# Kernel optimization log

Measured on AMD Instinct MI355X. Metric: run time of the kernel, lower is better.

Reference implementation:

```python
import jax, jax.numpy as jnp
import numpy as np

ALPHA = 0.9        # LIF membrane decay
THRESH = 1.0       # spike threshold
SURR_BETA = 4.0    # surrogate-gradient sharpness
TIME_STEPS = 32    # fabric simulation steps per token position


def _spike(v):
    """Heaviside spike with sigmoid surrogate gradient (straight-through)."""
    hard = (v >= THRESH).astype(v.dtype)
    soft = jax.nn.sigmoid(SURR_BETA * (v - THRESH))
    return soft + jax.lax.stop_gradient(hard - soft)


def setup_inputs() -> dict:
    key = jax.random.key(0)
    k0, k1, k2, k3 = jax.random.split(key, 4)
    B, S, D = 8, 128, 512
    N_in, N_out = 1024, 1024
    embeddings = jax.random.normal(k0, (B, S, D), jnp.float32)
    W_in = jax.random.normal(k1, (D, N_in), jnp.float32) / np.sqrt(D).astype(np.float32)
    b_in = jnp.zeros((N_in,), jnp.float32)
    W_conn = jax.random.normal(k2, (N_in, N_out), jnp.float32) / np.sqrt(N_in).astype(np.float32)
    W_out = jax.random.normal(k3, (N_out, D), jnp.float32) / np.sqrt(N_out).astype(np.float32)
    b_out = jnp.zeros((D,), jnp.float32)
    return {"embeddings": embeddings, "W_in": W_in, "b_in": b_in,
            "W_conn": W_conn, "W_out": W_out, "b_out": b_out}


def reference(embeddings, W_in, b_in, W_conn, W_out, b_out):
    B, S, D = embeddings.shape
    N_in = W_in.shape[1]
    N_out = W_conn.shape[1]

    # embed_to_snn + relu, precomputed for all positions: [B, S, N_in]
    snn_input = jax.nn.relu(jnp.einsum('bsd,dn->bsn', embeddings, W_in) + b_in)

    def time_step(carry, _):
        v_in, v_out, pos_input = carry
        # input population: leaky integrate external current
        v_in = ALPHA * v_in + pos_input
        s_in = _spike(v_in)
        v_in = v_in - s_in * THRESH          # soft reset
        # output population: driven by input-population spikes
        v_out = ALPHA * v_out + s_in @ W_conn
        s_out = _spike(v_out)
        v_out = v_out - s_out * THRESH
        n_spk = jax.lax.stop_gradient(s_in.sum() + s_out.sum())
        return (v_in, v_out, pos_input), (s_out, n_spk)

    def pos_step(carry, pos_input):
        v_in, v_out = carry
        (v_in, v_out, _), (s_outs, n_spks) = jax.lax.scan(
            time_step, (v_in, v_out, pos_input), None, length=TIME_STEPS)
        spike_acc = s_outs.sum(axis=0)       # [B, N_out], sum over timesteps
        pos_out = spike_acc @ W_out + b_out  # snn_to_embed
        return (v_in, v_out), (pos_out, n_spks.sum())

    v0_in = jnp.zeros((B, N_in), embeddings.dtype)
    v0_out = jnp.zeros((B, N_out), embeddings.dtype)
    snn_seq = jnp.swapaxes(snn_input, 0, 1)  # [S, B, N_in]: scan over positions
    _, (outs, spk_counts) = jax.lax.scan(pos_step, (v0_in, v0_out), snn_seq)

    output_embeddings = jnp.swapaxes(outs, 0, 1)  # [B, S, D]
    total_neurons = N_in + N_out
    spike_rate = spk_counts.sum() / (B * S * total_neurons * TIME_STEPS)
    return output_embeddings, spike_rate
```

## Files before the change

### kernel.cpp

```cpp
#include <hip/hip_runtime.h>
#include <stdint.h>

#define B 8
#define S 128
#define D 512
#define NIN 1024
#define NOUT 1024
#define T 32

typedef __attribute__((ext_vector_type(8))) short short8;
typedef __attribute__((ext_vector_type(4))) float floatx4;

__global__ __launch_bounds__(256) void k_gemm(const float* __restrict__ A,
                                              const float* __restrict__ Bm,
                                              const float* __restrict__ bias,
                                              float* __restrict__ C,
                                              int M, int N, int K, int relu)
{
    __shared__ float As[16][64];
    __shared__ float Bs[16][64];
    const int tid = threadIdx.x;
    const int bx = blockIdx.x, by = blockIdx.y;
    const int tx = tid & 15, ty = tid >> 4;
    const int ar = tid >> 2, ak = (tid & 3) << 2;
    const int bk = tid >> 4, bc = (tid & 15) << 2;
    float acc[4][4] = {{0.f,0.f,0.f,0.f},{0.f,0.f,0.f,0.f},
                       {0.f,0.f,0.f,0.f},{0.f,0.f,0.f,0.f}};
    for (int k0 = 0; k0 < K; k0 += 16) {
        float4 a4 = *(const float4*)(A + (size_t)(by*64 + ar)*K + k0 + ak);
        float4 b4 = *(const float4*)(Bm + (size_t)(k0 + bk)*N + bx*64 + bc);
        __syncthreads();
        As[ak+0][ar] = a4.x; As[ak+1][ar] = a4.y;
        As[ak+2][ar] = a4.z; As[ak+3][ar] = a4.w;
        *(float4*)&Bs[bk][bc] = b4;
        __syncthreads();
        #pragma unroll
        for (int kk = 0; kk < 16; ++kk) {
            float4 av = *(const float4*)&As[kk][ty << 2];
            float4 bv = *(const float4*)&Bs[kk][tx << 2];
            acc[0][0] = fmaf(av.x, bv.x, acc[0][0]);
            acc[0][1] = fmaf(av.x, bv.y, acc[0][1]);
            acc[0][2] = fmaf(av.x, bv.z, acc[0][2]);
            acc[0][3] = fmaf(av.x, bv.w, acc[0][3]);
            acc[1][0] = fmaf(av.y, bv.x, acc[1][0]);
            acc[1][1] = fmaf(av.y, bv.y, acc[1][1]);
            acc[1][2] = fmaf(av.y, bv.z, acc[1][2]);
            acc[1][3] = fmaf(av.y, bv.w, acc[1][3]);
            acc[2][0] = fmaf(av.z, bv.x, acc[2][0]);
            acc[2][1] = fmaf(av.z, bv.y, acc[2][1]);
            acc[2][2] = fmaf(av.z, bv.z, acc[2][2]);
            acc[2][3] = fmaf(av.z, bv.w, acc[2][3]);
            acc[3][0] = fmaf(av.w, bv.x, acc[3][0]);
            acc[3][1] = fmaf(av.w, bv.y, acc[3][1]);
            acc[3][2] = fmaf(av.w, bv.z, acc[3][2]);
            acc[3][3] = fmaf(av.w, bv.w, acc[3][3]);
        }
    }
    const int row0 = by*64 + (ty << 2), col0 = bx*64 + (tx << 2);
    float4 bb = *(const float4*)(bias + col0);
    #pragma unroll
    for (int i = 0; i < 4; ++i) {
        float4 o;
        o.x = acc[i][0] + bb.x; o.y = acc[i][1] + bb.y;
        o.z = acc[i][2] + bb.z; o.w = acc[i][3] + bb.w;
        if (relu) {
            o.x = fmaxf(o.x, 0.f); o.y = fmaxf(o.y, 0.f);
            o.z = fmaxf(o.z, 0.f); o.w = fmaxf(o.w, 0.f);
        }
        *(float4*)(C + (size_t)(row0 + i)*N + col0) = o;
    }
}

__global__ __launch_bounds__(256) void k_lif_inA(const float* __restrict__ snn,
                                                 unsigned int* __restrict__ sbits,
                                                 unsigned int* __restrict__ counters)
{
    const int tid = blockIdx.x * 256 + threadIdx.x;
    const int b = tid >> 10, n = tid & (NIN - 1);
    const float* cur = snn + (size_t)(b * S) * NIN + n;
    float v = 0.f;
    int cnt = 0;
    float I = cur[0];
    for (int s = 0; s < S; ++s) {
        const float In = (s + 1 < S) ? cur[(size_t)(s + 1) * NIN] : 0.f;
        unsigned int bits = 0u;
        #pragma unroll
        for (int t = 0; t < T; ++t) {
            v = __fadd_rn(__fmul_rn(0.9f, v), I);
            const bool sp = (v >= 1.0f);
            v = sp ? (v - 1.0f) : v;
            bits |= (sp ? 1u : 0u) << t;
        }
        sbits[(size_t)(b * S + s) * NIN + n] = bits;
        cnt += __popc(bits);
        I = In;
    }
    atomicAdd(counters, (unsigned int)cnt);
}

__global__ __launch_bounds__(256) void k_lif_inB(const unsigned int* __restrict__ sbits,
                                                 unsigned long long* __restrict__ masks)
{
    const int bs = blockIdx.x;
    const int w = threadIdx.x >> 6, lane = threadIdx.x & 63;
    #pragma unroll
    for (int i = 0; i < 4; ++i) {
        const int wq = w * 4 + i;
        const unsigned int bits = sbits[(size_t)bs * NIN + wq * 64 + lane];
        #pragma unroll
        for (int t = 0; t < T; ++t) {
            const unsigned long long m = __ballot((bits >> t) & 1u);
            if (lane == 0)
                masks[((size_t)bs * T + t) * 16 + wq] = m;
        }
    }
}

__global__ __launch_bounds__(256) void k_prep(const float* __restrict__ Wc,
                                              unsigned short* __restrict__ WhT,
                                              unsigned short* __restrict__ WlT)
{
    __shared__ float tile[64][65];
    const int k0 = blockIdx.x * 64, n0 = blockIdx.y * 64;
    const int tx = threadIdx.x & 63, ty = threadIdx.x >> 6;
    #pragma unroll
    for (int p = 0; p < 16; ++p) {
        const int kl = p*4 + ty;
        tile[kl][tx] = Wc[(size_t)(k0 + kl) * NOUT + n0 + tx];
    }
    __syncthreads();
    #pragma unroll
    for (int p = 0; p < 16; ++p) {
        const int nl = p*4 + ty;
        const float w = tile[tx][nl];
        const unsigned int u  = __float_as_uint(w);
        const unsigned int hb = (u + 0x7FFFu + ((u >> 16) & 1u)) & 0xFFFF0000u;
        const float hif = __uint_as_float(hb);
        const float lo  = w - hif;
        const unsigned int ul = __float_as_uint(lo);
        const unsigned short lob = (unsigned short)((ul + 0x7FFFu + ((ul >> 16) & 1u)) >> 16);
        WhT[(size_t)(n0 + nl) * NIN + k0 + tx] = (unsigned short)(hb >> 16);
        WlT[(size_t)(n0 + nl) * NIN + k0 + tx] = lob;
    }
}

__global__ __launch_bounds__(256) void k_conn_mfma(const uint4* __restrict__ masks128,
                                                   const unsigned short* __restrict__ WhT,
                                                   const unsigned short* __restrict__ WlT,
                                                   float* __restrict__ Iout,
                                                   int s0, int P)
{
    __shared__ uint4 lut[256];
    __shared__ unsigned short Bsm[2][64][136];

    const int tid = threadIdx.x;
    {
        const unsigned int bb = (unsigned int)tid;
        unsigned int r[4];
        #pragma unroll
        for (int i = 0; i < 4; ++i) {
            const unsigned int b0 = (bb >> (2*i)) & 1u, b1 = (bb >> (2*i+1)) & 1u;
            r[i] = (b0 ? 0x3F80u : 0u) | (b1 ? 0x3F800000u : 0u);
        }
        lut[tid] = make_uint4(r[0], r[1], r[2], r[3]);
    }

    const int w = tid >> 6, lane = tid & 63;
    const int r16 = lane & 15, q = lane >> 4;
    const int PT = P * T;
    const int rowblk = blockIdx.x * 256 + w * 64;
    const int cb = blockIdx.y * 64;

    const uint4* aptr[4];
    #pragma unroll
    for (int f = 0; f < 4; ++f) {
        const int r = rowblk + f*16 + r16;
        const int b = r / PT;
        const int within = r - b * PT;
        const int grow = (b * S + s0) * T + within;
        aptr[f] = masks128 + (size_t)grow * 8;
    }

    const int sflat0 = tid;
    floatx4 acc[4][4];
    #pragma unroll
    for (int f = 0; f < 4; ++f)
        #pragma unroll
        for (int c = 0; c < 4; ++c)
            acc[f][c] = (floatx4){0.f, 0.f, 0.f, 0.f};

    for (int ch = 0; ch < 8; ++ch) {
        __syncthreads();
        #pragma unroll
        for (int i = 0; i < 8; ++i) {
            const int flat = sflat0 + i * 256;
            const int mat  = flat >> 10;
            const int rest = flat & 1023;
            const int col  = rest >> 4;
            const int k16  = rest & 15;
            const unsigned short* src =
                (mat ? WlT : WhT) + (size_t)(cb + col) * NIN + ch * 128 + k16 * 8;
            *(uint4*)&Bsm[mat][col][k16 * 8] = *(const uint4*)src;
        }
        uint4 aw[4];
        #pragma unroll
        for (int f = 0; f < 4; ++f) aw[f] = aptr[f][ch];
        __syncthreads();

        #pragma unroll
        for (int kc = 0; kc < 4; ++kc) {
            short8 bh[4], bl[4];
            #pragma unroll
            for (int c = 0; c < 4; ++c) {
                bh[c] = *(const short8*)&Bsm[0][c*16 + r16][kc*32 + q*8];
                bl[c] = *(const short8*)&Bsm[1][c*16 + r16][kc*32 + q*8];
            }
            #pragma unroll
            for (int f = 0; f < 4; ++f) {
                const unsigned int word = (kc == 0) ? aw[f].x : (kc == 1) ? aw[f].y
                                         : (kc == 2) ? aw[f].z : aw[f].w;
                const unsigned int byte = (word >> (q * 8)) & 0xFFu;
                const short8 a = *(const short8*)&lut[byte];
                #pragma unroll
                for (int c = 0; c < 4; ++c) {
                    acc[f][c] = __builtin_amdgcn_mfma_f32_16x16x32_bf16(a, bh[c], acc[f][c], 0, 0, 0);
                    acc[f][c] = __builtin_amdgcn_mfma_f32_16x16x32_bf16(a, bl[c], acc[f][c], 0, 0, 0);
                }
            }
        }
    }

    #pragma unroll
    for (int f = 0; f < 4; ++f) {
        const int row = rowblk + f*16 + q*4;
        #pragma unroll
        for (int c = 0; c < 4; ++c) {
            const int col = cb + c*16 + r16;
            #pragma unroll
            for (int i = 0; i < 4; ++i)
                Iout[(size_t)(row + i) * NOUT + col] = acc[f][c][i];
        }
    }
}

__global__ __launch_bounds__(256) void k_lif_out(const float* __restrict__ Iout,
                                                 float* __restrict__ vstate,
                                                 float* __restrict__ sacc_out,
                                                 unsigned int* __restrict__ counters,
                                                 int s0, int P, int init)
{
    const int tid = blockIdx.x * 256 + threadIdx.x;
    const int b = tid >> 10, n = tid & (NOUT - 1);
    const int Tc = P * T;
    float v = init ? 0.f : vstate[tid];
    const float* ip = Iout + (size_t)b * Tc * NOUT + n;
    int cnt = 0;

    float cur[T];
    #pragma unroll
    for (int t = 0; t < T; ++t) cur[t] = ip[(size_t)t * NOUT];

    for (int sl = 0; sl < P; ++sl) {
        float nxt[T];
        const bool has = (sl + 1 < P);
        if (has) {
            const float* ip2 = ip + (size_t)(sl + 1) * T * NOUT;
            #pragma unroll
            for (int t = 0; t < T; ++t) nxt[t] = ip2[(size_t)t * NOUT];
        }
        float sacc = 0.f;
        #pragma unroll
        for (int t = 0; t < T; ++t) {
            v = __fadd_rn(__fmul_rn(0.9f, v), cur[t]);
            const bool sp = (v >= 1.0f);
            v = sp ? (v - 1.0f) : v;
            sacc += sp ? 1.f : 0.f;
            cnt += sp ? 1 : 0;
        }
        sacc_out[(size_t)(b*S + s0 + sl) * NOUT + n] = sacc;
        if (has) {
            #pragma unroll
            for (int t = 0; t < T; ++t) cur[t] = nxt[t];
        }
    }
    vstate[tid] = v;
    atomicAdd(counters + 1, (unsigned int)cnt);
}

__global__ void k_init(unsigned int* c)
{
    if (threadIdx.x < 2) c[threadIdx.x] = 0u;
}

__global__ void k_rate(const unsigned int* __restrict__ c, float* __restrict__ out)
{
    if (threadIdx.x == 0 && blockIdx.x == 0) {
        const float total = (float)c[0] + (float)c[1];
        out[0] = total / (float)(B * S * (NIN + NOUT) * T);
    }
}

extern "C" void kernel_launch(void* const* d_in, const int* in_sizes, int n_in,
                              void* d_out, int out_size, void* d_ws, size_t ws_size,
                              hipStream_t stream)
{
    const float* E    = (const float*)d_in[0];
    const float* Win  = (const float*)d_in[1];
    const float* bin  = (const float*)d_in[2];
    const float* Wc   = (const float*)d_in[3];
    const float* Wout = (const float*)d_in[4];
    const float* bout = (const float*)d_in[5];
    float* out = (float*)d_out;

    char* w = (char*)d_ws;
    float* snn              = (float*)(w);
    unsigned short* WhT     = (unsigned short*)(w);
    unsigned short* WlT     = (unsigned short*)(w + (2 << 20));
    unsigned long long* msk = (unsigned long long*)(w + (4 << 20));
    float* sacc             = (float*)(w + (8 << 20));
    unsigned int* sbits     = (unsigned int*)(w + (8 << 20));
    float* vst              = (float*)(w + (12 << 20));
    unsigned int* cnt       = (unsigned int*)(w + (12 << 20) + (64 << 10));
    float* Iout             = (float*)(w + (13 << 20));

    const size_t base = (size_t)13 << 20;
    const size_t avail = (ws_size > base) ? (ws_size - base) : 0;
    int P = 1;
    if      (avail >= (size_t)B * 128 * T * NOUT * 4) P = 128;
    else if (avail >= (size_t)B *  16 * T * NOUT * 4) P = 16;
    else if (avail >= (size_t)B *   4 * T * NOUT * 4) P = 4;

    k_init<<<1, 64, 0, stream>>>(cnt);

    dim3 g1(NIN / 64, (B * S) / 64);
    k_gemm<<<g1, 256, 0, stream>>>(E, Win, bin, snn, B * S, NIN, D, 1);

    k_lif_inA<<<32, 256, 0, stream>>>(snn, sbits, cnt);
    k_lif_inB<<<B * S, 256, 0, stream>>>(sbits, msk);

    dim3 gp(NIN / 64, NOUT / 64);
    k_prep<<<gp, 256, 0, stream>>>(Wc, WhT, WlT);

    for (int c = 0; c < S / P; ++c) {
        dim3 gc((B * P * T) / 256, NOUT / 64);
        k_conn_mfma<<<gc, 256, 0, stream>>>((const uint4*)msk, WhT, WlT, Iout, c * P, P);
        k_lif_out<<<32, 256, 0, stream>>>(Iout, vst, sacc, cnt, c * P, P, c == 0 ? 1 : 0);
    }

    dim3 g2(D / 64, (B * S) / 64);
    k_gemm<<<g2, 256, 0, stream>>>(sacc, Wout, bout, out, B * S, D, NOUT, 0);

    k_rate<<<1, 64, 0, stream>>>(cnt, out + (size_t)B * S * D);
}
```

Measured before the change: 473.4 us.

## Retile spike-weight GEMM to 256x128 blocks with 32x32 MFMA and register prefetch

The spike-mask times W_conn GEMM is restructured. Each block now covers a 256x128 output tile with a 2x2 wave layout and uses 32x32x16 bf16 MFMAs. Spike bits are expanded to bf16 with arithmetic and staged in shared memory instead of through a per-lane LUT. The next K-chunk of masks and weights is prefetched into registers while the current chunk runs through the MFMAs. This aims to raise arithmetic intensity and cut redundant mask and weight loads, at the cost of higher register and LDS pressure (64KB of shared memory, launch bounds of 2 blocks).

After: 568.7 us. 20.1% more time.

```diff
diff --git a/kernel.cpp b/kernel.cpp
--- a/kernel.cpp
+++ b/kernel.cpp
@@ -10,6 +10,7 @@
 
 typedef __attribute__((ext_vector_type(8))) short short8;
 typedef __attribute__((ext_vector_type(4))) float floatx4;
+typedef __attribute__((ext_vector_type(16))) float floatx16;
 
 __global__ __launch_bounds__(256) void k_gemm(const float* __restrict__ A,
                                               const float* __restrict__ Bm,
@@ -144,101 +145,111 @@
     }
 }
 
-__global__ __launch_bounds__(256) void k_conn_mfma(const uint4* __restrict__ masks128,
-                                                   const unsigned short* __restrict__ WhT,
-                                                   const unsigned short* __restrict__ WlT,
-                                                   float* __restrict__ Iout,
-                                                   int s0, int P)
-{
-    __shared__ uint4 lut[256];
-    __shared__ unsigned short Bsm[2][64][136];
+__global__ __launch_bounds__(256, 2) void k_conn_mfma(
+    const unsigned long long* __restrict__ masks64,
+    const unsigned short* __restrict__ WhT,
+    const unsigned short* __restrict__ WlT,
+    float* __restrict__ Iout, int s0, int P)
+{
+    __shared__ unsigned short sm[32768];
 
     const int tid = threadIdx.x;
-    {
-        const unsigned int bb = (unsigned int)tid;
-        unsigned int r[4];
-        #pragma unroll
-        for (int i = 0; i < 4; ++i) {
-            const unsigned int b0 = (bb >> (2*i)) & 1u, b1 = (bb >> (2*i+1)) & 1u;
-            r[i] = (b0 ? 0x3F80u : 0u) | (b1 ? 0x3F800000u : 0u);
-        }
-        lut[tid] = make_uint4(r[0], r[1], r[2], r[3]);
-    }
-
     const int w = tid >> 6, lane = tid & 63;
-    const int r16 = lane & 15, q = lane >> 4;
+    const int wr = w >> 1, wc = w & 1;
+    const int l31 = lane & 31, q8 = lane >> 5;
     const int PT = P * T;
-    const int rowblk = blockIdx.x * 256 + w * 64;
-    const int cb = blockIdx.y * 64;
-
-    const uint4* aptr[4];
+    const int rowblk = blockIdx.x * 256;
+    const int cb = blockIdx.y * 128;
+
+    const int r = rowblk + tid;
+    const int rb = r / PT;
+    const int grow = rb * (S * T) + s0 * T + (r - rb * PT);
+    const unsigned long long* mrow = masks64 + (size_t)grow * 16;
+    const int fg = tid >> 5;
+    const int m31 = tid & 31;
+
+    const unsigned short* bsrc[8];
+    unsigned short* bdst[8];
+    #pragma unroll
+    for (int i = 0; i < 8; ++i) {
+        const int slot = w * 8 + i;
+        const int mat = slot >> 4, rest = slot & 15;
+        const int cfrag = rest >> 2, k16 = rest & 3;
+        bsrc[i] = (mat ? WlT : WhT)
+                + (size_t)(cb + cfrag * 32 + l31) * NIN + k16 * 16 + q8 * 8;
+        bdst[i] = sm + 16384 + slot * 512 + lane * 8;
+    }
+
+    floatx16 acc[4][2];
+    #pragma unroll
+    for (int f = 0; f < 4; ++f)
+        #pragma unroll
+        for (int c = 0; c < 2; ++c)
+            acc[f][c] = (floatx16){0.f,0.f,0.f,0.f,0.f,0.f,0.f,0.f,
+                                   0.f,0.f,0.f,0.f,0.f,0.f,0.f,0.f};
+
+    unsigned long long mv = mrow[0];
+    uint4 bw[8];
+    #pragma unroll
+    for (int i = 0; i < 8; ++i) bw[i] = *(const uint4*)(bsrc[i]);
+
+    for (int ch = 0; ch < 16; ++ch) {
+        __syncthreads();
+        #pragma unroll
+        for (int k16 = 0; k16 < 4; ++k16)
+            #pragma unroll
+            for (int q = 0; q < 2; ++q) {
+                const unsigned int by = (unsigned int)(mv >> (k16 * 16 + q * 8)) & 0xFFu;
+                uint4 dv;
+                dv.x = (((by >> 0) & 1u) | (((by >> 1) & 1u) << 16)) * 0x3F80u;
+                dv.y = (((by >> 2) & 1u) | (((by >> 3) & 1u) << 16)) * 0x3F80u;
+                dv.z = (((by >> 4) & 1u) | (((by >> 5) & 1u) << 16)) * 0x3F80u;
+                dv.w = (((by >> 6) & 1u) | (((by >> 7) & 1u) << 16)) * 0x3F80u;
+                *(uint4*)&sm[(fg * 4 + k16) * 512 + (m31 + 32 * q) * 8] = dv;
+            }
+        #pragma unroll
+        for (int i = 0; i < 8; ++i) *(uint4*)bdst[i] = bw[i];
+        __syncthreads();
+
+        if (ch + 1 < 16) {
+            mv = mrow[ch + 1];
+            #pragma unroll
+            for (int i = 0; i < 8; ++i)
+                bw[i] = *(const uint4*)(bsrc[i] + (ch + 1) * 64);
+        }
+
+        #pragma unroll
+        for (int k16 = 0; k16 < 4; ++k16) {
+            short8 af[4], bh[2], bl[2];
+            #pragma unroll
+            for (int f = 0; f < 4; ++f)
+                af[f] = *(const short8*)&sm[((wr * 4 + f) * 4 + k16) * 512 + lane * 8];
+            #pragma unroll
+            for (int c = 0; c < 2; ++c) {
+                bh[c] = *(const short8*)&sm[16384 + (((wc * 2 + c) * 4) + k16) * 512 + lane * 8];
+                bl[c] = *(const short8*)&sm[16384 + ((16 + (wc * 2 + c) * 4) + k16) * 512 + lane * 8];
+            }
+            #pragma unroll
+            for (int f = 0; f < 4; ++f)
+                #pragma unroll
+                for (int c = 0; c < 2; ++c) {
+                    acc[f][c] = __builtin_amdgcn_mfma_f32_32x32x16_bf16(af[f], bh[c], acc[f][c], 0, 0, 0);
+                    acc[f][c] = __builtin_amdgcn_mfma_f32_32x32x16_bf16(af[f], bl[c], acc[f][c], 0, 0, 0);
+                }
+        }
+    }
+
     #pragma unroll
     for (int f = 0; f < 4; ++f) {
-        const int r = rowblk + f*16 + r16;
-        const int b = r / PT;
-        const int within = r - b * PT;
-        const int grow = (b * S + s0) * T + within;
-        aptr[f] = masks128 + (size_t)grow * 8;
-    }
-
-    const int sflat0 = tid;
-    floatx4 acc[4][4];
-    #pragma unroll
-    for (int f = 0; f < 4; ++f)
-        #pragma unroll
-        for (int c = 0; c < 4; ++c)
-            acc[f][c] = (floatx4){0.f, 0.f, 0.f, 0.f};
-
-    for (int ch = 0; ch < 8; ++ch) {
-        __syncthreads();
-        #pragma unroll
-        for (int i = 0; i < 8; ++i) {
-            const int flat = sflat0 + i * 256;
-            const int mat  = flat >> 10;
-            const int rest = flat & 1023;
-            const int col  = rest >> 4;
-            const int k16  = rest & 15;
-            const unsigned short* src =
-                (mat ? WlT : WhT) + (size_t)(cb + col) * NIN + ch * 128 + k16 * 8;
-            *(uint4*)&Bsm[mat][col][k16 * 8] = *(const uint4*)src;
-        }
-        uint4 aw[4];
-        #pragma unroll
-        for (int f = 0; f < 4; ++f) aw[f] = aptr[f][ch];
-        __syncthreads();
-
-        #pragma unroll
-        for (int kc = 0; kc < 4; ++kc) {
-            short8 bh[4], bl[4];
-            #pragma unroll
-            for (int c = 0; c < 4; ++c) {
-                bh[c] = *(const short8*)&Bsm[0][c*16 + r16][kc*32 + q*8];
-                bl[c] = *(const short8*)&Bsm[1][c*16 + r16][kc*32 + q*8];
+        const int row0 = rowblk + wr * 128 + f * 32 + 4 * q8;
+        #pragma unroll
+        for (int c = 0; c < 2; ++c) {
+            const int col = cb + wc * 64 + c * 32 + l31;
+            #pragma unroll
+            for (int i = 0; i < 16; ++i) {
+                const int row = row0 + (i & 3) + 8 * (i >> 2);
+                Iout[(size_t)row * NOUT + col] = acc[f][c][i];
             }
-            #pragma unroll
-            for (int f = 0; f < 4; ++f) {
-                const unsigned int word = (kc == 0) ? aw[f].x : (kc == 1) ? aw[f].y
-                                         : (kc == 2) ? aw[f].z : aw[f].w;
-                const unsigned int byte = (word >> (q * 8)) & 0xFFu;
-                const short8 a = *(const short8*)&lut[byte];
-                #pragma unroll
-                for (int c = 0; c < 4; ++c) {
-                    acc[f][c] = __builtin_amdgcn_mfma_f32_16x16x32_bf16(a, bh[c], acc[f][c], 0, 0, 0);
-                    acc[f][c] = __builtin_amdgcn_mfma_f32_16x16x32_bf16(a, bl[c], acc[f][c], 0, 0, 0);
-                }
-            }
-        }
-    }
-
-    #pragma unroll
-    for (int f = 0; f < 4; ++f) {
-        const int row = rowblk + f*16 + q*4;
-        #pragma unroll
-        for (int c = 0; c < 4; ++c) {
-            const int col = cb + c*16 + r16;
-            #pragma unroll
-            for (int i = 0; i < 4; ++i)
-                Iout[(size_t)(row + i) * NOUT + col] = acc[f][c][i];
         }
     }
 }
@@ -342,8 +353,8 @@
     k_prep<<<gp, 256, 0, stream>>>(Wc, WhT, WlT);
 
     for (int c = 0; c < S / P; ++c) {
-        dim3 gc((B * P * T) / 256, NOUT / 64);
-        k_conn_mfma<<<gc, 256, 0, stream>>>((const uint4*)msk, WhT, WlT, Iout, c * P, P);
+        dim3 gc((B * P * T) / 256, NOUT / 128);
+        k_conn_mfma<<<gc, 256, 0, stream>>>(msk, WhT, WlT, Iout, c * P, P);
         k_lif_out<<<32, 256, 0, stream>>>(Iout, vst, sacc, cnt, c * P, P, c == 0 ? 1 : 0);
     }
 
```

## Widen conn MFMA tile to 128 columns with fragment-ordered LDS layout

Applied to the files above, without the earlier changes.

Doubles the output-column tile per block of the spike-by-weight MFMA kernel from 64 to 128, so each A fragment is reused across 8 column fragments and the grid halves. The weight tiles are staged in shared memory in a fragment-contiguous layout with precomputed offsets, which removes strided, padded LDS reads. The spike-mask bf16 fragments are now built in registers instead of through a shared lookup table. The accumulator doubles to 128 floats per thread, which raises register pressure, and launch_bounds(256,2) is added to keep two blocks per CU.

New measurement: 493.8 us. 4.3% more time.

```diff
diff --git a/kernel.cpp b/kernel.cpp
--- a/kernel.cpp
+++ b/kernel.cpp
@@ -144,32 +144,20 @@
     }
 }
 
-__global__ __launch_bounds__(256) void k_conn_mfma(const uint4* __restrict__ masks128,
-                                                   const unsigned short* __restrict__ WhT,
-                                                   const unsigned short* __restrict__ WlT,
-                                                   float* __restrict__ Iout,
-                                                   int s0, int P)
-{
-    __shared__ uint4 lut[256];
-    __shared__ unsigned short Bsm[2][64][136];
+__global__ __launch_bounds__(256, 2) void k_conn_mfma(
+    const uint4* __restrict__ masks128,
+    const unsigned short* __restrict__ WhT,
+    const unsigned short* __restrict__ WlT,
+    float* __restrict__ Iout, int s0, int P)
+{
+    __shared__ unsigned short Bsm[2 * 4 * 8 * 512];
 
     const int tid = threadIdx.x;
-    {
-        const unsigned int bb = (unsigned int)tid;
-        unsigned int r[4];
-        #pragma unroll
-        for (int i = 0; i < 4; ++i) {
-            const unsigned int b0 = (bb >> (2*i)) & 1u, b1 = (bb >> (2*i+1)) & 1u;
-            r[i] = (b0 ? 0x3F80u : 0u) | (b1 ? 0x3F800000u : 0u);
-        }
-        lut[tid] = make_uint4(r[0], r[1], r[2], r[3]);
-    }
-
     const int w = tid >> 6, lane = tid & 63;
     const int r16 = lane & 15, q = lane >> 4;
     const int PT = P * T;
     const int rowblk = blockIdx.x * 256 + w * 64;
-    const int cb = blockIdx.y * 64;
+    const int cb = blockIdx.y * 128;
 
     const uint4* aptr[4];
     #pragma unroll
@@ -181,27 +169,36 @@
         aptr[f] = masks128 + (size_t)grow * 8;
     }
 
-    const int sflat0 = tid;
-    floatx4 acc[4][4];
+    const int lane_s = tid & 63, s0slot = tid >> 6;
+    unsigned int boff[16];
+    #pragma unroll
+    for (int i = 0; i < 16; ++i) {
+        const int slot = s0slot + 4 * i;
+        const int cfrag = slot & 7, kc = (slot >> 3) & 3;
+        boff[i] = (unsigned int)((cfrag * 16 + (lane_s & 15)) * NIN
+                                 + kc * 32 + (lane_s >> 4) * 8);
+    }
+    const unsigned short* whb = WhT + (size_t)cb * NIN;
+    const unsigned short* wlb = WlT + (size_t)cb * NIN;
+    unsigned short* bdst = Bsm + 8 * tid;
+
+    floatx4 acc[4][8];
     #pragma unroll
     for (int f = 0; f < 4; ++f)
         #pragma unroll
-        for (int c = 0; c < 4; ++c)
+        for (int c = 0; c < 8; ++c)
             acc[f][c] = (floatx4){0.f, 0.f, 0.f, 0.f};
+
+    const unsigned short* bp = Bsm + (size_t)lane * 8;
 
     for (int ch = 0; ch < 8; ++ch) {
         __syncthreads();
         #pragma unroll
-        for (int i = 0; i < 8; ++i) {
-            const int flat = sflat0 + i * 256;
-            const int mat  = flat >> 10;
-            const int rest = flat & 1023;
-            const int col  = rest >> 4;
-            const int k16  = rest & 15;
-            const unsigned short* src =
-                (mat ? WlT : WhT) + (size_t)(cb + col) * NIN + ch * 128 + k16 * 8;
-            *(uint4*)&Bsm[mat][col][k16 * 8] = *(const uint4*)src;
-        }
+        for (int i = 0; i < 8; ++i)
+            *(uint4*)(bdst + i * 2048) = *(const uint4*)(whb + boff[i] + ch * 128);
+        #pragma unroll
+        for (int i = 8; i < 16; ++i)
+            *(uint4*)(bdst + i * 2048) = *(const uint4*)(wlb + boff[i] + ch * 128);
         uint4 aw[4];
         #pragma unroll
         for (int f = 0; f < 4; ++f) aw[f] = aptr[f][ch];
@@ -209,22 +206,27 @@
 
         #pragma unroll
         for (int kc = 0; kc < 4; ++kc) {
-            short8 bh[4], bl[4];
-            #pragma unroll
-            for (int c = 0; c < 4; ++c) {
-                bh[c] = *(const short8*)&Bsm[0][c*16 + r16][kc*32 + q*8];
-                bl[c] = *(const short8*)&Bsm[1][c*16 + r16][kc*32 + q*8];
-            }
+            short8 af[4];
             #pragma unroll
             for (int f = 0; f < 4; ++f) {
                 const unsigned int word = (kc == 0) ? aw[f].x : (kc == 1) ? aw[f].y
                                          : (kc == 2) ? aw[f].z : aw[f].w;
                 const unsigned int byte = (word >> (q * 8)) & 0xFFu;
-                const short8 a = *(const short8*)&lut[byte];
+                union { unsigned int u[4]; short8 s; } A;
                 #pragma unroll
-                for (int c = 0; c < 4; ++c) {
-                    acc[f][c] = __builtin_amdgcn_mfma_f32_16x16x32_bf16(a, bh[c], acc[f][c], 0, 0, 0);
-                    acc[f][c] = __builtin_amdgcn_mfma_f32_16x16x32_bf16(a, bl[c], acc[f][c], 0, 0, 0);
+                for (int j = 0; j < 4; ++j)
+                    A.u[j] = (((byte >> (2*j)) & 1u) ? 0x3F80u : 0u)
+                           | (((byte >> (2*j+1)) & 1u) ? 0x3F800000u : 0u);
+                af[f] = A.s;
+            }
+            #pragma unroll
+            for (int c = 0; c < 8; ++c) {
+                const short8 bh = *(const short8*)(bp + ((kc * 8 + c) << 9));
+                const short8 bl = *(const short8*)(bp + ((32 * 512) + ((kc * 8 + c) << 9)));
+                #pragma unroll
+                for (int f = 0; f < 4; ++f) {
+                    acc[f][c] = __builtin_amdgcn_mfma_f32_16x16x32_bf16(af[f], bh, acc[f][c], 0, 0, 0);
+                    acc[f][c] = __builtin_amdgcn_mfma_f32_16x16x32_bf16(af[f], bl, acc[f][c], 0, 0, 0);
                 }
             }
         }
@@ -234,7 +236,7 @@
     for (int f = 0; f < 4; ++f) {
         const int row = rowblk + f*16 + q*4;
         #pragma unroll
-        for (int c = 0; c < 4; ++c) {
+        for (int c = 0; c < 8; ++c) {
             const int col = cb + c*16 + r16;
             #pragma unroll
             for (int i = 0; i < 4; ++i)
@@ -342,7 +344,7 @@
     k_prep<<<gp, 256, 0, stream>>>(Wc, WhT, WlT);
 
     for (int c = 0; c < S / P; ++c) {
-        dim3 gc((B * P * T) / 256, NOUT / 64);
+        dim3 gc((B * P * T) / 256, NOUT / 128);
         k_conn_mfma<<<gc, 256, 0, stream>>>((const uint4*)msk, WhT, WlT, Iout, c * P, P);
         k_lif_out<<<32, 256, 0, stream>>>(Iout, vst, sacc, cnt, c * P, P, c == 0 ? 1 : 0);
     }
```
